# Optimization experiments

Measured on AMD Instinct MI355X. Metric: run time of the kernel, lower is better.

## Reference

```python
import jax, jax.numpy as jnp
import numpy as np

DIM, HEADS, DIM_HEAD = 512, 8, 64

def setup_inputs() -> dict:
    key = jax.random.key(0)
    ks = jax.random.split(key, 9)
    B, T = 4, 4096
    s = 1.0 / np.sqrt(DIM)
    x = jax.random.normal(ks[0], (B, T, DIM), dtype=jnp.float32)
    Wq = jax.random.uniform(ks[1], (DIM, DIM), jnp.float32, -s, s)
    Wk = jax.random.uniform(ks[2], (DIM, DIM), jnp.float32, -s, s)
    Wv = jax.random.uniform(ks[3], (DIM, DIM), jnp.float32, -s, s)
    Wp = jax.random.uniform(ks[4], (DIM, DIM), jnp.float32, -s, s)
    bq = jax.random.uniform(ks[5], (DIM,), jnp.float32, -s, s)
    bk = jax.random.uniform(ks[6], (DIM,), jnp.float32, -s, s)
    bv = jax.random.uniform(ks[7], (DIM,), jnp.float32, -s, s)
    bp = jax.random.uniform(ks[8], (DIM,), jnp.float32, -s, s)
    return {"x": x, "Wq": Wq, "bq": bq, "Wk": Wk, "bk": bk,
            "Wv": Wv, "bv": bv, "Wp": Wp, "bp": bp}

def reference(x, Wq, bq, Wk, bk, Wv, bv, Wp, bp):
    B, T, _ = x.shape
    H, D = HEADS, DIM_HEAD
    # projections -> [B, H, T, D]
    def proj(W, b):
        return (x @ W.T + b).reshape(B, T, H, D).transpose(0, 2, 1, 3)
    q = jax.nn.softmax(proj(Wq, bq), axis=-1)
    k = jax.nn.softmax(proj(Wk, bk), axis=-1)
    v = proj(Wv, bv)
    # l1 normalization: D_inv = 1 / <q, sum_t k>
    k_sum = k.sum(axis=2, keepdims=True)                 # [B,H,1,D]
    D_inv = 1.0 / (q * k_sum).sum(axis=-1, keepdims=True)  # [B,H,T,1]
    context = jnp.einsum('bhtd,bhte->bhde', k, v)        # small DxD per head
    out = jnp.einsum('bhtd,bhde->bhte', q, context) * D_inv + q
    out = out.transpose(0, 2, 1, 3).reshape(B, T, H * D)
    return out @ Wp.T + bp
```

## Files before the change

kernel.cpp:

```cpp
#include <hip/hip_runtime.h>

#define NTOK  16384
#define KDIM  512
#define NQKV  1536
#define TT    4096

using frag8   = __attribute__((ext_vector_type(8))) short;
using floatx4 = __attribute__((ext_vector_type(4))) float;

__device__ __forceinline__ unsigned short f2b(float f) {
  union { float f; unsigned u; } v; v.f = f;
  unsigned r = v.u + 0x7fffu + ((v.u >> 16) & 1u);
  return (unsigned short)(r >> 16);
}
__device__ __forceinline__ float b2f(unsigned short s) {
  union { unsigned u; float f; } v; v.u = ((unsigned)s) << 16; return v.f;
}
__device__ __forceinline__ float blo(unsigned w) {
  union { unsigned u; float f; } v; v.u = w << 16; return v.f;
}
__device__ __forceinline__ float bhi(unsigned w) {
  union { unsigned u; float f; } v; v.u = w & 0xffff0000u; return v.f;
}

__device__ __forceinline__ void gl_lds16(const void* g, void* l) {
  __builtin_amdgcn_global_load_lds((__attribute__((address_space(1))) const void*)g,
                                   (__attribute__((address_space(3))) void*)l,
                                   16, 0, 0);
}

__global__ __launch_bounds__(256) void cvt_x(const float* __restrict__ x,
                                             unsigned short* __restrict__ xb) {
  const size_t i = (size_t)blockIdx.x * 256 + threadIdx.x;
  const float4 v = ((const float4*)x)[i];
  ushort4 o;
  o.x = f2b(v.x); o.y = f2b(v.y); o.z = f2b(v.z); o.w = f2b(v.w);
  ((ushort4*)xb)[i] = o;
}

__global__ __launch_bounds__(256) void prep_weights(
    const float* __restrict__ Wq, const float* __restrict__ Wk,
    const float* __restrict__ Wv, const float* __restrict__ Wp,
    const float* __restrict__ bq, const float* __restrict__ bk,
    const float* __restrict__ bv,
    unsigned short* __restrict__ wqkv, unsigned short* __restrict__ wp,
    float* __restrict__ bias_qkv) {
  const int idx = blockIdx.x * 256 + threadIdx.x;
  if (idx < 786432) {
    const int m = idx >> 9, i = idx & 511;
    const float* W = (m < 512) ? Wq : ((m < 1024) ? Wk : Wv);
    wqkv[idx] = f2b(W[(m & 511) * 512 + i]);
    return;
  }
  const int j = idx - 786432;
  if (j < 262144) { wp[j] = f2b(Wp[j]); return; }
  const int c = j - 262144;
  if (c < 1536)
    bias_qkv[c] = (c < 512) ? bq[c] : ((c < 1024) ? bk[c - 512] : bv[c - 1024]);
}

template<int SOFT>
__global__ __launch_bounds__(256, 2) void gemm_bt(
    const unsigned short* __restrict__ A,
    const unsigned short* __restrict__ Bm,
    const float* __restrict__ bias,
    void* __restrict__ C,
    int M, int N, int K, int ldc)
{
  __shared__ unsigned short sh[2 * 128 * 32];
  unsigned short* As = sh;
  unsigned short* Bs = sh + 128 * 32;
  const int tid  = threadIdx.x;
  const int wave = tid >> 6;
  const int lane = tid & 63;
  const int quad = lane >> 4;
  const int lr   = lane & 15;
  const int bid  = ((blockIdx.x & 7) * (gridDim.x >> 3)) + (blockIdx.x >> 3);
  const int nt   = N >> 7;
  const int bn   = (bid % nt) << 7;
  const int bm   = (bid / nt) << 7;
  const int half = wave >> 1;
  const int wm   = half << 6;
  const int wn   = (wave & 1) << 6;

  floatx4 acc[4][4] = {};

  const int srow = tid >> 2;
  const int scol = (tid & 3) << 3;
  const unsigned short* Ag = A + (size_t)(bm + srow) * K + scol;
  const unsigned short* Bg = Bm + (size_t)(bn + srow) * K + scol;
  unsigned short* Al = As + (wave << 9);
  unsigned short* Bl = Bs + (wave << 9);

  for (int k0 = 0; k0 < K; k0 += 32) {
    __syncthreads();
    gl_lds16(Ag + k0, Al);
    gl_lds16(Ag + (size_t)64 * K + k0, Al + 64 * 32);
    gl_lds16(Bg + k0, Bl);
    gl_lds16(Bg + (size_t)64 * K + k0, Bl + 64 * 32);
    __syncthreads();

    frag8 af[4], bf[4];
#pragma unroll
    for (int i = 0; i < 4; i++)
      af[i] = *(const frag8*)&As[(wm + (i << 4) + lr) * 32 + (quad << 3)];
#pragma unroll
    for (int j = 0; j < 4; j++)
      bf[j] = *(const frag8*)&Bs[(wn + (j << 4) + lr) * 32 + (quad << 3)];
#pragma unroll
    for (int i = 0; i < 4; i++)
#pragma unroll
      for (int j = 0; j < 4; j++)
        acc[i][j] = __builtin_amdgcn_mfma_f32_16x16x32_bf16(af[i], bf[j], acc[i][j], 0, 0, 0);
  }

  const int ccol0 = bn + wn + lr;

#pragma unroll
  for (int j = 0; j < 4; j++) {
    const float bv = bias[ccol0 + (j << 4)];
#pragma unroll
    for (int i = 0; i < 4; i++)
#pragma unroll
      for (int r = 0; r < 4; r++)
        acc[i][j][r] += bv;
  }

  if (SOFT) {
    const int region = (bn + wn) >> 9;
    if (region < 2) {
#pragma unroll
      for (int i = 0; i < 4; i++)
#pragma unroll
        for (int r = 0; r < 4; r++) {
          float e0 = __expf(acc[i][0][r]);
          float e1 = __expf(acc[i][1][r]);
          float e2 = __expf(acc[i][2][r]);
          float e3 = __expf(acc[i][3][r]);
          float s = e0 + e1 + e2 + e3;
          s += __shfl_xor(s, 1);
          s += __shfl_xor(s, 2);
          s += __shfl_xor(s, 4);
          s += __shfl_xor(s, 8);
          const float inv = 1.f / s;
          acc[i][0][r] = e0 * inv; acc[i][1][r] = e1 * inv;
          acc[i][2][r] = e2 * inv; acc[i][3][r] = e3 * inv;
        }
    }
    unsigned short* os = sh;
#pragma unroll
    for (int p = 0; p < 2; p++) {
      __syncthreads();
      if (half == p) {
#pragma unroll
        for (int i = 0; i < 4; i++)
#pragma unroll
          for (int j = 0; j < 4; j++)
#pragma unroll
            for (int r = 0; r < 4; r++)
              os[((i << 4) + (quad << 2) + r) * 128 + wn + (j << 4) + lr] = f2b(acc[i][j][r]);
      }
      __syncthreads();
#pragma unroll
      for (int it = 0; it < 4; it++) {
        const int idx = (it << 8) + tid;
        const int row = idx >> 4;
        const int c8  = (idx & 15) << 3;
        *(uint4*)((unsigned short*)C + (size_t)(bm + (p << 6) + row) * ldc + bn + c8) =
            *(const uint4*)&os[row * 128 + c8];
      }
    }
  } else {
    const int crow0 = bm + wm + (quad << 2);
#pragma unroll
    for (int j = 0; j < 4; j++) {
      const int col = ccol0 + (j << 4);
#pragma unroll
      for (int i = 0; i < 4; i++) {
        const int row = crow0 + (i << 4);
#pragma unroll
        for (int r = 0; r < 4; r++)
          ((float*)C)[(size_t)(row + r) * ldc + col] = acc[i][j][r];
      }
    }
  }
}

__global__ __launch_bounds__(256) void kv_context(const unsigned short* __restrict__ qkv,
                                                  float* __restrict__ part,
                                                  float* __restrict__ ksp) {
  const int bid = blockIdx.x;
  const int tc  = bid & 31;
  const int bh  = bid >> 5;
  const int b   = bh >> 3, h = bh & 7;
  __shared__ float ks[16 * 64];
  __shared__ float vs[16 * 64];
  const int tid = threadIdx.x;
  const int ty = tid >> 4, tx = tid & 15;
  floatx4 acc[4] = {};
  floatx4 ksacc = {0.f, 0.f, 0.f, 0.f};

  const int si    = tid << 3;
  const int strow = si >> 7;
  const int sw    = si & 127;
  const int t0    = b * TT + tc * 128;
  const unsigned short* gcol = qkv + ((sw < 64) ? (512 + h * 64 + sw)
                                                : (1024 + h * 64 + (sw - 64)));
  float* sdst = (sw < 64) ? &ks[strow * 64 + sw] : &vs[strow * 64 + (sw - 64)];

  for (int tt = 0; tt < 128; tt += 16) {
    __syncthreads();
    const uint4 raw = *(const uint4*)(gcol + (size_t)(t0 + tt + strow) * NQKV);
    sdst[0] = blo(raw.x); sdst[1] = bhi(raw.x);
    sdst[2] = blo(raw.y); sdst[3] = bhi(raw.y);
    sdst[4] = blo(raw.z); sdst[5] = bhi(raw.z);
    sdst[6] = blo(raw.w); sdst[7] = bhi(raw.w);
    __syncthreads();
#pragma unroll
    for (int t = 0; t < 16; t++) {
      const floatx4 vb = *(const floatx4*)&vs[t * 64 + (ty << 2)];
      const floatx4 kb = *(const floatx4*)&ks[t * 64 + (tx << 2)];
      acc[0] += vb.x * kb;
      acc[1] += vb.y * kb;
      acc[2] += vb.z * kb;
      acc[3] += vb.w * kb;
    }
    ksacc += *(const floatx4*)&ks[ty * 64 + (tx << 2)];
  }
  __syncthreads();
  *(floatx4*)&vs[ty * 64 + (tx << 2)] = ksacc;
  __syncthreads();

  float* pg = part + ((size_t)(tc * 32 + bh) << 12) + (size_t)(ty << 2) * 64 + (tx << 2);
#pragma unroll
  for (int i = 0; i < 4; i++)
    *(floatx4*)(pg + i * 64) = acc[i];

  if (tid < 64) {
    float s = 0.f;
    for (int t2 = 0; t2 < 16; t2++) s += vs[t2 * 64 + tid];
    ksp[(tc * 32 + bh) * 64 + tid] = s;
  }
}

__global__ __launch_bounds__(256) void ctx_reduce(const float* __restrict__ part,
                                                  const float* __restrict__ ksp,
                                                  unsigned short* __restrict__ ctxb) {
  const int bh = blockIdx.x / 20, g = blockIdx.x % 20;
  const int row = (g << 2) + (threadIdx.x >> 6);
  const int d   = threadIdx.x & 63;
  float s = 0.f;
  if (row < 64) {
    const float* p = part + ((size_t)bh << 12) + row * 64 + d;
    for (int c = 0; c < 32; c++) s += p[(size_t)c << 17];
  } else if (row == 64) {
    const float* p = ksp + bh * 64 + d;
    for (int c = 0; c < 32; c++) s += p[c << 11];
  }
  ctxb[(size_t)bh * 5120 + (row << 6) + d] = f2b(s);
}

__global__ __launch_bounds__(256) void attn_out(const unsigned short* __restrict__ qkv,
                                                const unsigned short* __restrict__ ctxb,
                                                unsigned short* __restrict__ opre) {
  const int bid = blockIdx.x;
  const int tc = bid & 63;
  const int bh = bid >> 6;
  const int b = bh >> 3, h = bh & 7;
  const int t0 = b * TT + (tc << 6);
  __shared__ unsigned short sh[144 * 72];
  unsigned short* qs = sh;
  unsigned short* cs = sh + 64 * 72;
  unsigned short* os = cs;
  const int tid = threadIdx.x;

  for (int i = tid; i < 512; i += 256) {
    const int row = i >> 3, c8 = (i & 7) << 3;
    *(uint4*)&qs[row * 72 + c8] =
        *(const uint4*)&qkv[(size_t)(t0 + row) * NQKV + h * 64 + c8];
  }
  for (int i = tid; i < 640; i += 256) {
    const int row = i >> 3, c8 = (i & 7) << 3;
    *(uint4*)&cs[row * 72 + c8] =
        *(const uint4*)&ctxb[(size_t)bh * 5120 + (row << 6) + c8];
  }
  __syncthreads();

  const int lane = tid & 63, w = tid >> 6, quad = lane >> 4, lr = lane & 15;
  floatx4 acc[5] = {};
#pragma unroll
  for (int k2 = 0; k2 < 2; k2++) {
    const int d0 = (k2 << 5) + (quad << 3);
    const frag8 bf = *(const frag8*)&qs[((w << 4) + lr) * 72 + d0];
#pragma unroll
    for (int et = 0; et < 5; et++) {
      const frag8 af = *(const frag8*)&cs[(et * 16 + lr) * 72 + d0];
      acc[et] = __builtin_amdgcn_mfma_f32_16x16x32_bf16(af, bf, acc[et], 0, 0, 0);
    }
  }
  const float dinv = 1.f / __shfl(acc[4][0], lr);
  __syncthreads();

  const int trow = (w << 4) + lr;
#pragma unroll
  for (int et = 0; et < 4; et++)
#pragma unroll
    for (int r = 0; r < 4; r++) {
      const int e = et * 16 + (quad << 2) + r;
      const float qv = b2f(qs[trow * 72 + e]);
      os[trow * 72 + e] = f2b(acc[et][r] * dinv + qv);
    }
  __syncthreads();

  for (int i = tid; i < 512; i += 256) {
    const int row = i >> 3, c8 = (i & 7) << 3;
    *(uint4*)&opre[(size_t)(t0 + row) * KDIM + h * 64 + c8] = *(const uint4*)&os[row * 72 + c8];
  }
}

extern "C" void kernel_launch(void* const* d_in, const int* in_sizes, int n_in,
                              void* d_out, int out_size, void* d_ws, size_t ws_size,
                              hipStream_t stream) {
  (void)in_sizes; (void)n_in; (void)out_size; (void)ws_size;
  const float* x  = (const float*)d_in[0];
  const float* Wq = (const float*)d_in[1];
  const float* bq = (const float*)d_in[2];
  const float* Wk = (const float*)d_in[3];
  const float* bk = (const float*)d_in[4];
  const float* Wv = (const float*)d_in[5];
  const float* bv = (const float*)d_in[6];
  const float* Wp = (const float*)d_in[7];
  const float* bp = (const float*)d_in[8];

  char* w = (char*)d_ws;
  unsigned short* xb   = (unsigned short*)w; w += (size_t)NTOK * KDIM * 2;
  float* part          = (float*)xb;
  unsigned short* wqkv = (unsigned short*)w; w += (size_t)NQKV * KDIM * 2;
  unsigned short* wp   = (unsigned short*)w; w += (size_t)KDIM * KDIM * 2;
  float* bias_qkv      = (float*)w;          w += (size_t)NQKV * 4;
  float* ksp           = (float*)w;          w += (size_t)1024 * 64 * 4;
  unsigned short* ctxb = (unsigned short*)w; w += (size_t)32 * 80 * 64 * 2;
  unsigned short* qkv  = (unsigned short*)w; w += (size_t)NTOK * NQKV * 2;
  unsigned short* opre = (unsigned short*)w; w += (size_t)NTOK * KDIM * 2;

  cvt_x<<<8192, 256, 0, stream>>>(x, xb);
  prep_weights<<<4102, 256, 0, stream>>>(Wq, Wk, Wv, Wp, bq, bk, bv, wqkv, wp, bias_qkv);
  gemm_bt<1><<<(NTOK / 128) * (NQKV / 128), 256, 0, stream>>>(
      xb, wqkv, bias_qkv, qkv, NTOK, NQKV, KDIM, NQKV);
  kv_context<<<1024, 256, 0, stream>>>(qkv, part, ksp);
  ctx_reduce<<<640, 256, 0, stream>>>(part, ksp, ctxb);
  attn_out<<<2048, 256, 0, stream>>>(qkv, ctxb, opre);
  gemm_bt<0><<<(NTOK / 128) * (KDIM / 128), 256, 0, stream>>>(
      opre, wp, bp, d_out, NTOK, KDIM, KDIM, KDIM);
}
```

Before: 192.7 us.

## Enlarge QKV GEMM tile, async-load K/V in bf16, vectorize reduce, drop LDS staging in attn_out

The QKV GEMM moves to a 256x128 block tile in which each wave computes 64x128, so the softmax covers two heads per wave and each LDS-staged tile is reused more. kv_context now fetches K/V straight into LDS as bf16 with global_load_lds and converts at use time, instead of converting to fp32 in registers first. ctx_reduce uses float4 loads with a quarter of the blocks. attn_out reads Q and the context directly from global memory without staging them in LDS, and reorders blocks so that heads are interleaved. gemm_out hardcodes its dimensions. The larger accumulator raises register pressure, and the bf16 rounding of the output before the q add changes precision slightly.

```diff
diff --git a/kernel.cpp b/kernel.cpp
--- a/kernel.cpp
+++ b/kernel.cpp
@@ -15,12 +15,6 @@
 }
 __device__ __forceinline__ float b2f(unsigned short s) {
   union { unsigned u; float f; } v; v.u = ((unsigned)s) << 16; return v.f;
-}
-__device__ __forceinline__ float blo(unsigned w) {
-  union { unsigned u; float f; } v; v.u = w << 16; return v.f;
-}
-__device__ __forceinline__ float bhi(unsigned w) {
-  union { unsigned u; float f; } v; v.u = w & 0xffff0000u; return v.f;
 }
 
 __device__ __forceinline__ void gl_lds16(const void* g, void* l) {
@@ -59,13 +53,254 @@
     bias_qkv[c] = (c < 512) ? bq[c] : ((c < 1024) ? bk[c - 512] : bv[c - 1024]);
 }
 
-template<int SOFT>
-__global__ __launch_bounds__(256, 2) void gemm_bt(
+__global__ __launch_bounds__(256, 2) void gemm_qkv(
     const unsigned short* __restrict__ A,
     const unsigned short* __restrict__ Bm,
     const float* __restrict__ bias,
-    void* __restrict__ C,
-    int M, int N, int K, int ldc)
+    unsigned short* __restrict__ C)
+{
+  __shared__ unsigned short sh[128 * 128];
+  unsigned short* As = sh;
+  unsigned short* Bs = sh + 256 * 32;
+  const int tid  = threadIdx.x;
+  const int wave = tid >> 6;
+  const int lane = tid & 63;
+  const int quad = lane >> 4;
+  const int lr   = lane & 15;
+  const int bid  = ((blockIdx.x & 7) * 96) + (blockIdx.x >> 3);
+  const int bn   = (bid % 12) << 7;
+  const int bm   = (bid / 12) << 8;
+  const int wm   = wave << 6;
+
+  floatx4 acc[4][8] = {};
+
+  const int srow = tid >> 2;
+  const int scol = (tid & 3) << 3;
+  const unsigned short* Ag = A + (size_t)(bm + srow) * 512 + scol;
+  const unsigned short* Bg = Bm + (size_t)(bn + srow) * 512 + scol;
+  unsigned short* Al = As + (wave << 9);
+  unsigned short* Bl = Bs + (wave << 9);
+
+  for (int k0 = 0; k0 < 512; k0 += 32) {
+    __syncthreads();
+    gl_lds16(Ag + k0, Al);
+    gl_lds16(Ag + 64 * 512 + k0, Al + 64 * 32);
+    gl_lds16(Ag + 128 * 512 + k0, Al + 128 * 32);
+    gl_lds16(Ag + 192 * 512 + k0, Al + 192 * 32);
+    gl_lds16(Bg + k0, Bl);
+    gl_lds16(Bg + 64 * 512 + k0, Bl + 64 * 32);
+    __syncthreads();
+
+    frag8 af[4], bf[8];
+#pragma unroll
+    for (int i = 0; i < 4; i++)
+      af[i] = *(const frag8*)&As[(wm + (i << 4) + lr) * 32 + (quad << 3)];
+#pragma unroll
+    for (int j = 0; j < 8; j++)
+      bf[j] = *(const frag8*)&Bs[((j << 4) + lr) * 32 + (quad << 3)];
+#pragma unroll
+    for (int i = 0; i < 4; i++)
+#pragma unroll
+      for (int j = 0; j < 8; j++)
+        acc[i][j] = __builtin_amdgcn_mfma_f32_16x16x32_bf16(af[i], bf[j], acc[i][j], 0, 0, 0);
+  }
+
+  const int ccol0 = bn + lr;
+#pragma unroll
+  for (int j = 0; j < 8; j++) {
+    const float bv = bias[ccol0 + (j << 4)];
+#pragma unroll
+    for (int i = 0; i < 4; i++)
+#pragma unroll
+      for (int r = 0; r < 4; r++)
+        acc[i][j][r] += bv;
+  }
+
+  const int region = bn >> 9;
+  if (region < 2) {
+#pragma unroll
+    for (int i = 0; i < 4; i++)
+#pragma unroll
+      for (int r = 0; r < 4; r++) {
+        float e0 = __expf(acc[i][0][r]);
+        float e1 = __expf(acc[i][1][r]);
+        float e2 = __expf(acc[i][2][r]);
+        float e3 = __expf(acc[i][3][r]);
+        float e4 = __expf(acc[i][4][r]);
+        float e5 = __expf(acc[i][5][r]);
+        float e6 = __expf(acc[i][6][r]);
+        float e7 = __expf(acc[i][7][r]);
+        float sl = e0 + e1 + e2 + e3;
+        float sg = e4 + e5 + e6 + e7;
+        sl += __shfl_xor(sl, 1); sl += __shfl_xor(sl, 2);
+        sl += __shfl_xor(sl, 4); sl += __shfl_xor(sl, 8);
+        sg += __shfl_xor(sg, 1); sg += __shfl_xor(sg, 2);
+        sg += __shfl_xor(sg, 4); sg += __shfl_xor(sg, 8);
+        const float il = 1.f / sl, ig = 1.f / sg;
+        acc[i][0][r] = e0 * il; acc[i][1][r] = e1 * il;
+        acc[i][2][r] = e2 * il; acc[i][3][r] = e3 * il;
+        acc[i][4][r] = e4 * ig; acc[i][5][r] = e5 * ig;
+        acc[i][6][r] = e6 * ig; acc[i][7][r] = e7 * ig;
+      }
+  }
+
+  unsigned short* os = sh;
+#pragma unroll
+  for (int p = 0; p < 2; p++) {
+    __syncthreads();
+    if ((wave >> 1) == p) {
+      const int rb = (wave & 1) << 6;
+#pragma unroll
+      for (int i = 0; i < 4; i++)
+#pragma unroll
+        for (int j = 0; j < 8; j++)
+#pragma unroll
+          for (int r = 0; r < 4; r++)
+            os[(rb + (i << 4) + (quad << 2) + r) * 128 + (j << 4) + lr] = f2b(acc[i][j][r]);
+    }
+    __syncthreads();
+#pragma unroll
+    for (int it = 0; it < 8; it++) {
+      const int idx = (it << 8) + tid;
+      const int row = idx >> 4;
+      const int c8  = (idx & 15) << 3;
+      *(uint4*)(C + (size_t)(bm + (p << 7) + row) * NQKV + bn + c8) =
+          *(const uint4*)&os[row * 128 + c8];
+    }
+  }
+}
+
+__global__ __launch_bounds__(256) void kv_context(const unsigned short* __restrict__ qkv,
+                                                  float* __restrict__ part,
+                                                  float* __restrict__ ksp) {
+  const int bid = blockIdx.x;
+  const int tc  = bid & 31;
+  const int bh  = bid >> 5;
+  const int b   = bh >> 3, h = bh & 7;
+  __shared__ unsigned short kb16[16 * 64];
+  __shared__ unsigned short vb16[16 * 64];
+  __shared__ float ksred[16 * 64];
+  const int tid = threadIdx.x;
+  const int wave = tid >> 6;
+  const int lane = tid & 63;
+  const int ty = tid >> 4, tx = tid & 15;
+  floatx4 acc[4] = {};
+  floatx4 ksacc = {0.f, 0.f, 0.f, 0.f};
+
+  const int t0 = b * TT + tc * 128;
+  const int kvsel = wave >> 1;
+  const int rowb  = (wave & 1) << 3;
+  const unsigned short* gsrc = qkv + (size_t)(t0 + rowb + (lane >> 3)) * NQKV
+                               + 512 + (kvsel << 9) + h * 64 + ((lane & 7) << 3);
+  unsigned short* ldst = (kvsel ? vb16 : kb16) + (rowb << 6);
+
+  for (int tt = 0; tt < 128; tt += 16) {
+    __syncthreads();
+    gl_lds16(gsrc + (size_t)tt * NQKV, ldst);
+    __syncthreads();
+#pragma unroll
+    for (int t = 0; t < 16; t++) {
+      const ushort4 kr = *(const ushort4*)&kb16[t * 64 + (tx << 2)];
+      const ushort4 vr = *(const ushort4*)&vb16[t * 64 + (ty << 2)];
+      floatx4 kf;
+      kf.x = b2f(kr.x); kf.y = b2f(kr.y); kf.z = b2f(kr.z); kf.w = b2f(kr.w);
+      acc[0] += b2f(vr.x) * kf;
+      acc[1] += b2f(vr.y) * kf;
+      acc[2] += b2f(vr.z) * kf;
+      acc[3] += b2f(vr.w) * kf;
+    }
+    const ushort4 kk = *(const ushort4*)&kb16[ty * 64 + (tx << 2)];
+    ksacc.x += b2f(kk.x); ksacc.y += b2f(kk.y);
+    ksacc.z += b2f(kk.z); ksacc.w += b2f(kk.w);
+  }
+  __syncthreads();
+  *(floatx4*)&ksred[ty * 64 + (tx << 2)] = ksacc;
+  __syncthreads();
+
+  float* pg = part + ((size_t)(tc * 32 + bh) << 12) + (size_t)(ty << 2) * 64 + (tx << 2);
+#pragma unroll
+  for (int i = 0; i < 4; i++)
+    *(floatx4*)(pg + i * 64) = acc[i];
+
+  if (tid < 64) {
+    float s = 0.f;
+    for (int t2 = 0; t2 < 16; t2++) s += ksred[t2 * 64 + tid];
+    ksp[(tc * 32 + bh) * 64 + tid] = s;
+  }
+}
+
+__global__ __launch_bounds__(256) void ctx_reduce(const float* __restrict__ part,
+                                                  const float* __restrict__ ksp,
+                                                  unsigned short* __restrict__ ctxb) {
+  const int bh = blockIdx.x / 5, g = blockIdx.x % 5;
+  const int row = (g << 4) + (threadIdx.x >> 4);
+  const int d0  = (threadIdx.x & 15) << 2;
+  floatx4 s = {0.f, 0.f, 0.f, 0.f};
+  if (row < 64) {
+    const float* p = part + ((size_t)bh << 12) + row * 64 + d0;
+    for (int c = 0; c < 32; c++)
+      s += *(const floatx4*)(p + ((size_t)c << 17));
+  } else if (row == 64) {
+    const float* p = ksp + bh * 64 + d0;
+    for (int c = 0; c < 32; c++)
+      s += *(const floatx4*)(p + (c << 11));
+  }
+  ushort4 o;
+  o.x = f2b(s.x); o.y = f2b(s.y); o.z = f2b(s.z); o.w = f2b(s.w);
+  *(ushort4*)&ctxb[(size_t)bh * 5120 + (row << 6) + d0] = o;
+}
+
+__global__ __launch_bounds__(256) void attn_out(const unsigned short* __restrict__ qkv,
+                                                const unsigned short* __restrict__ ctxb,
+                                                unsigned short* __restrict__ opre) {
+  const int tc = blockIdx.x >> 5;
+  const int bh = blockIdx.x & 31;
+  const int b = bh >> 3, h = bh & 7;
+  const int t0 = b * TT + (tc << 6);
+  __shared__ unsigned short os[64 * 72];
+  const int tid = threadIdx.x;
+  const int lane = tid & 63, w = tid >> 6, quad = lane >> 4, lr = lane & 15;
+
+  floatx4 acc[5] = {};
+  const unsigned short* qbase = qkv + (size_t)(t0 + (w << 4) + lr) * NQKV + h * 64 + (quad << 3);
+  const unsigned short* cbase = ctxb + (size_t)bh * 5120 + (quad << 3);
+#pragma unroll
+  for (int k2 = 0; k2 < 2; k2++) {
+    const frag8 bfr = *(const frag8*)(qbase + (k2 << 5));
+#pragma unroll
+    for (int et = 0; et < 5; et++) {
+      const frag8 afr = *(const frag8*)(cbase + (((et << 4) + lr) << 6) + (k2 << 5));
+      acc[et] = __builtin_amdgcn_mfma_f32_16x16x32_bf16(afr, bfr, acc[et], 0, 0, 0);
+    }
+  }
+  const float dinv = 1.f / __shfl(acc[4][0], lr);
+
+  const int trow = (w << 4) + lr;
+#pragma unroll
+  for (int et = 0; et < 4; et++)
+#pragma unroll
+    for (int r = 0; r < 4; r++)
+      os[trow * 72 + (et << 4) + (quad << 2) + r] = f2b(acc[et][r] * dinv);
+  __syncthreads();
+
+  for (int i = tid; i < 512; i += 256) {
+    const int row = i >> 3, c8 = (i & 7) << 3;
+    const uint4 qraw = *(const uint4*)&qkv[(size_t)(t0 + row) * NQKV + h * 64 + c8];
+    const uint4 ov   = *(const uint4*)&os[row * 72 + c8];
+    const unsigned short* qp = (const unsigned short*)&qraw;
+    const unsigned short* op = (const unsigned short*)&ov;
+    unsigned short o8[8];
+#pragma unroll
+    for (int jj = 0; jj < 8; jj++) o8[jj] = f2b(b2f(op[jj]) + b2f(qp[jj]));
+    *(uint4*)&opre[(size_t)(t0 + row) * KDIM + h * 64 + c8] = *(const uint4*)o8;
+  }
+}
+
+__global__ __launch_bounds__(256, 2) void gemm_out(
+    const unsigned short* __restrict__ A,
+    const unsigned short* __restrict__ Bm,
+    const float* __restrict__ bias,
+    float* __restrict__ C)
 {
   __shared__ unsigned short sh[2 * 128 * 32];
   unsigned short* As = sh;
@@ -75,29 +310,27 @@
   const int lane = tid & 63;
   const int quad = lane >> 4;
   const int lr   = lane & 15;
-  const int bid  = ((blockIdx.x & 7) * (gridDim.x >> 3)) + (blockIdx.x >> 3);
-  const int nt   = N >> 7;
-  const int bn   = (bid % nt) << 7;
-  const int bm   = (bid / nt) << 7;
-  const int half = wave >> 1;
-  const int wm   = half << 6;
+  const int bid  = ((blockIdx.x & 7) * 64) + (blockIdx.x >> 3);
+  const int bn   = (bid & 3) << 7;
+  const int bm   = (bid >> 2) << 7;
+  const int wm   = (wave >> 1) << 6;
   const int wn   = (wave & 1) << 6;
 
   floatx4 acc[4][4] = {};
 
   const int srow = tid >> 2;
   const int scol = (tid & 3) << 3;
-  const unsigned short* Ag = A + (size_t)(bm + srow) * K + scol;
-  const unsigned short* Bg = Bm + (size_t)(bn + srow) * K + scol;
+  const unsigned short* Ag = A + (size_t)(bm + srow) * 512 + scol;
+  const unsigned short* Bg = Bm + (size_t)(bn + srow) * 512 + scol;
   unsigned short* Al = As + (wave << 9);
   unsigned short* Bl = Bs + (wave << 9);
 
-  for (int k0 = 0; k0 < K; k0 += 32) {
+  for (int k0 = 0; k0 < 512; k0 += 32) {
     __syncthreads();
     gl_lds16(Ag + k0, Al);
-    gl_lds16(Ag + (size_t)64 * K + k0, Al + 64 * 32);
+    gl_lds16(Ag + 64 * 512 + k0, Al + 64 * 32);
     gl_lds16(Bg + k0, Bl);
-    gl_lds16(Bg + (size_t)64 * K + k0, Bl + 64 * 32);
+    gl_lds16(Bg + 64 * 512 + k0, Bl + 64 * 32);
     __syncthreads();
 
     frag8 af[4], bf[4];
@@ -114,207 +347,19 @@
         acc[i][j] = __builtin_amdgcn_mfma_f32_16x16x32_bf16(af[i], bf[j], acc[i][j], 0, 0, 0);
   }
 
+  const int crow0 = bm + wm + (quad << 2);
   const int ccol0 = bn + wn + lr;
-
 #pragma unroll
   for (int j = 0; j < 4; j++) {
-    const float bv = bias[ccol0 + (j << 4)];
-#pragma unroll
-    for (int i = 0; i < 4; i++)
+    const int col = ccol0 + (j << 4);
+    const float bv = bias[col];
+#pragma unroll
+    for (int i = 0; i < 4; i++) {
+      const int row = crow0 + (i << 4);
 #pragma unroll
       for (int r = 0; r < 4; r++)
-        acc[i][j][r] += bv;
-  }
-
-  if (SOFT) {
-    const int region = (bn + wn) >> 9;
-    if (region < 2) {
-#pragma unroll
-      for (int i = 0; i < 4; i++)
-#pragma unroll
-        for (int r = 0; r < 4; r++) {
-          float e0 = __expf(acc[i][0][r]);
-          float e1 = __expf(acc[i][1][r]);
-          float e2 = __expf(acc[i][2][r]);
-          float e3 = __expf(acc[i][3][r]);
-          float s = e0 + e1 + e2 + e3;
-          s += __shfl_xor(s, 1);
-          s += __shfl_xor(s, 2);
-          s += __shfl_xor(s, 4);
-          s += __shfl_xor(s, 8);
-          const float inv = 1.f / s;
-          acc[i][0][r] = e0 * inv; acc[i][1][r] = e1 * inv;
-          acc[i][2][r] = e2 * inv; acc[i][3][r] = e3 * inv;
-        }
-    }
-    unsigned short* os = sh;
-#pragma unroll
-    for (int p = 0; p < 2; p++) {
-      __syncthreads();
-      if (half == p) {
-#pragma unroll
-        for (int i = 0; i < 4; i++)
-#pragma unroll
-          for (int j = 0; j < 4; j++)
-#pragma unroll
-            for (int r = 0; r < 4; r++)
-              os[((i << 4) + (quad << 2) + r) * 128 + wn + (j << 4) + lr] = f2b(acc[i][j][r]);
-      }
-      __syncthreads();
-#pragma unroll
-      for (int it = 0; it < 4; it++) {
-        const int idx = (it << 8) + tid;
-        const int row = idx >> 4;
-        const int c8  = (idx & 15) << 3;
-        *(uint4*)((unsigned short*)C + (size_t)(bm + (p << 6) + row) * ldc + bn + c8) =
-            *(const uint4*)&os[row * 128 + c8];
-      }
-    }
-  } else {
-    const int crow0 = bm + wm + (quad << 2);
-#pragma unroll
-    for (int j = 0; j < 4; j++) {
-      const int col = ccol0 + (j << 4);
-#pragma unroll
-      for (int i = 0; i < 4; i++) {
-        const int row = crow0 + (i << 4);
-#pragma unroll
-        for (int r = 0; r < 4; r++)
-          ((float*)C)[(size_t)(row + r) * ldc + col] = acc[i][j][r];
-      }
-    }
-  }
-}
-
-__global__ __launch_bounds__(256) void kv_context(const unsigned short* __restrict__ qkv,
-                                                  float* __restrict__ part,
-                                                  float* __restrict__ ksp) {
-  const int bid = blockIdx.x;
-  const int tc  = bid & 31;
-  const int bh  = bid >> 5;
-  const int b   = bh >> 3, h = bh & 7;
-  __shared__ float ks[16 * 64];
-  __shared__ float vs[16 * 64];
-  const int tid = threadIdx.x;
-  const int ty = tid >> 4, tx = tid & 15;
-  floatx4 acc[4] = {};
-  floatx4 ksacc = {0.f, 0.f, 0.f, 0.f};
-
-  const int si    = tid << 3;
-  const int strow = si >> 7;
-  const int sw    = si & 127;
-  const int t0    = b * TT + tc * 128;
-  const unsigned short* gcol = qkv + ((sw < 64) ? (512 + h * 64 + sw)
-                                                : (1024 + h * 64 + (sw - 64)));
-  float* sdst = (sw < 64) ? &ks[strow * 64 + sw] : &vs[strow * 64 + (sw - 64)];
-
-  for (int tt = 0; tt < 128; tt += 16) {
-    __syncthreads();
-    const uint4 raw = *(const uint4*)(gcol + (size_t)(t0 + tt + strow) * NQKV);
-    sdst[0] = blo(raw.x); sdst[1] = bhi(raw.x);
-    sdst[2] = blo(raw.y); sdst[3] = bhi(raw.y);
-    sdst[4] = blo(raw.z); sdst[5] = bhi(raw.z);
-    sdst[6] = blo(raw.w); sdst[7] = bhi(raw.w);
-    __syncthreads();
-#pragma unroll
-    for (int t = 0; t < 16; t++) {
-      const floatx4 vb = *(const floatx4*)&vs[t * 64 + (ty << 2)];
-      const floatx4 kb = *(const floatx4*)&ks[t * 64 + (tx << 2)];
-      acc[0] += vb.x * kb;
-      acc[1] += vb.y * kb;
-      acc[2] += vb.z * kb;
-      acc[3] += vb.w * kb;
-    }
-    ksacc += *(const floatx4*)&ks[ty * 64 + (tx << 2)];
-  }
-  __syncthreads();
-  *(floatx4*)&vs[ty * 64 + (tx << 2)] = ksacc;
-  __syncthreads();
-
-  float* pg = part + ((size_t)(tc * 32 + bh) << 12) + (size_t)(ty << 2) * 64 + (tx << 2);
-#pragma unroll
-  for (int i = 0; i < 4; i++)
-    *(floatx4*)(pg + i * 64) = acc[i];
-
-  if (tid < 64) {
-    float s = 0.f;
-    for (int t2 = 0; t2 < 16; t2++) s += vs[t2 * 64 + tid];
-    ksp[(tc * 32 + bh) * 64 + tid] = s;
-  }
-}
-
-__global__ __launch_bounds__(256) void ctx_reduce(const float* __restrict__ part,
-                                                  const float* __restrict__ ksp,
-                                                  unsigned short* __restrict__ ctxb) {
-  const int bh = blockIdx.x / 20, g = blockIdx.x % 20;
-  const int row = (g << 2) + (threadIdx.x >> 6);
-  const int d   = threadIdx.x & 63;
-  float s = 0.f;
-  if (row < 64) {
-    const float* p = part + ((size_t)bh << 12) + row * 64 + d;
-    for (int c = 0; c < 32; c++) s += p[(size_t)c << 17];
-  } else if (row == 64) {
-    const float* p = ksp + bh * 64 + d;
-    for (int c = 0; c < 32; c++) s += p[c << 11];
-  }
-  ctxb[(size_t)bh * 5120 + (row << 6) + d] = f2b(s);
-}
-
-__global__ __launch_bounds__(256) void attn_out(const unsigned short* __restrict__ qkv,
-                                                const unsigned short* __restrict__ ctxb,
-                                                unsigned short* __restrict__ opre) {
-  const int bid = blockIdx.x;
-  const int tc = bid & 63;
-  const int bh = bid >> 6;
-  const int b = bh >> 3, h = bh & 7;
-  const int t0 = b * TT + (tc << 6);
-  __shared__ unsigned short sh[144 * 72];
-  unsigned short* qs = sh;
-  unsigned short* cs = sh + 64 * 72;
-  unsigned short* os = cs;
-  const int tid = threadIdx.x;
-
-  for (int i = tid; i < 512; i += 256) {
-    const int row = i >> 3, c8 = (i & 7) << 3;
-    *(uint4*)&qs[row * 72 + c8] =
-        *(const uint4*)&qkv[(size_t)(t0 + row) * NQKV + h * 64 + c8];
-  }
-  for (int i = tid; i < 640; i += 256) {
-    const int row = i >> 3, c8 = (i & 7) << 3;
-    *(uint4*)&cs[row * 72 + c8] =
-        *(const uint4*)&ctxb[(size_t)bh * 5120 + (row << 6) + c8];
-  }
-  __syncthreads();
-
-  const int lane = tid & 63, w = tid >> 6, quad = lane >> 4, lr = lane & 15;
-  floatx4 acc[5] = {};
-#pragma unroll
-  for (int k2 = 0; k2 < 2; k2++) {
-    const int d0 = (k2 << 5) + (quad << 3);
-    const frag8 bf = *(const frag8*)&qs[((w << 4) + lr) * 72 + d0];
-#pragma unroll
-    for (int et = 0; et < 5; et++) {
-      const frag8 af = *(const frag8*)&cs[(et * 16 + lr) * 72 + d0];
-      acc[et] = __builtin_amdgcn_mfma_f32_16x16x32_bf16(af, bf, acc[et], 0, 0, 0);
-    }
-  }
-  const float dinv = 1.f / __shfl(acc[4][0], lr);
-  __syncthreads();
-
-  const int trow = (w << 4) + lr;
-#pragma unroll
-  for (int et = 0; et < 4; et++)
-#pragma unroll
-    for (int r = 0; r < 4; r++) {
-      const int e = et * 16 + (quad << 2) + r;
-      const float qv = b2f(qs[trow * 72 + e]);
-      os[trow * 72 + e] = f2b(acc[et][r] * dinv + qv);
-    }
-  __syncthreads();
-
-  for (int i = tid; i < 512; i += 256) {
-    const int row = i >> 3, c8 = (i & 7) << 3;
-    *(uint4*)&opre[(size_t)(t0 + row) * KDIM + h * 64 + c8] = *(const uint4*)&os[row * 72 + c8];
+        C[(size_t)(row + r) * 512 + col] = acc[i][j][r] + bv;
+    }
   }
 }
 
@@ -345,11 +390,9 @@
 
   cvt_x<<<8192, 256, 0, stream>>>(x, xb);
   prep_weights<<<4102, 256, 0, stream>>>(Wq, Wk, Wv, Wp, bq, bk, bv, wqkv, wp, bias_qkv);
-  gemm_bt<1><<<(NTOK / 128) * (NQKV / 128), 256, 0, stream>>>(
-      xb, wqkv, bias_qkv, qkv, NTOK, NQKV, KDIM, NQKV);
+  gemm_qkv<<<768, 256, 0, stream>>>(xb, wqkv, bias_qkv, qkv);
   kv_context<<<1024, 256, 0, stream>>>(qkv, part, ksp);
-  ctx_reduce<<<640, 256, 0, stream>>>(part, ksp, ctxb);
+  ctx_reduce<<<160, 256, 0, stream>>>(part, ksp, ctxb);
   attn_out<<<2048, 256, 0, stream>>>(qkv, ctxb, opre);
-  gemm_bt<0><<<(NTOK / 128) * (KDIM / 128), 256, 0, stream>>>(
-      opre, wp, bp, d_out, NTOK, KDIM, KDIM, KDIM);
-}
+  gemm_out<<<512, 256, 0, stream>>>(opre, wp, bp, (float*)d_out);
+}
```

After: 205.5 us. +6.6%, slower.

## Stream K/V directly from global in kv_context, vectorize ctx_reduce, raise gemm occupancy

Applied to the files above, without the earlier changes.

kv_context drops its LDS staging and syncthreads. Each thread now loads its own 4-wide K and V bf16 slices straight from global memory and accumulates the outer product and the k-sum in registers. ctx_reduce becomes float4-vectorized with a quarter of the blocks, attn_out's block index mapping is changed to interleave heads, and the gemm launch bounds ask for 4 blocks per SM. These aim to cut sync overhead, raise memory throughput and improve occupancy. The costs are redundant global loads across threads in kv_context and register pressure in the gemm.

```diff
diff --git a/kernel.cpp b/kernel.cpp
--- a/kernel.cpp
+++ b/kernel.cpp
@@ -15,12 +15,6 @@
 }
 __device__ __forceinline__ float b2f(unsigned short s) {
   union { unsigned u; float f; } v; v.u = ((unsigned)s) << 16; return v.f;
-}
-__device__ __forceinline__ float blo(unsigned w) {
-  union { unsigned u; float f; } v; v.u = w << 16; return v.f;
-}
-__device__ __forceinline__ float bhi(unsigned w) {
-  union { unsigned u; float f; } v; v.u = w & 0xffff0000u; return v.f;
 }
 
 __device__ __forceinline__ void gl_lds16(const void* g, void* l) {
@@ -60,7 +54,7 @@
 }
 
 template<int SOFT>
-__global__ __launch_bounds__(256, 2) void gemm_bt(
+__global__ __launch_bounds__(256, 4) void gemm_bt(
     const unsigned short* __restrict__ A,
     const unsigned short* __restrict__ Bm,
     const float* __restrict__ bias,
@@ -189,83 +183,66 @@
 __global__ __launch_bounds__(256) void kv_context(const unsigned short* __restrict__ qkv,
                                                   float* __restrict__ part,
                                                   float* __restrict__ ksp) {
-  const int bid = blockIdx.x;
-  const int tc  = bid & 31;
-  const int bh  = bid >> 5;
+  const int tc  = blockIdx.x & 31;
+  const int bh  = blockIdx.x >> 5;
   const int b   = bh >> 3, h = bh & 7;
-  __shared__ float ks[16 * 64];
-  __shared__ float vs[16 * 64];
   const int tid = threadIdx.x;
   const int ty = tid >> 4, tx = tid & 15;
   floatx4 acc[4] = {};
   floatx4 ksacc = {0.f, 0.f, 0.f, 0.f};
 
-  const int si    = tid << 3;
-  const int strow = si >> 7;
-  const int sw    = si & 127;
-  const int t0    = b * TT + tc * 128;
-  const unsigned short* gcol = qkv + ((sw < 64) ? (512 + h * 64 + sw)
-                                                : (1024 + h * 64 + (sw - 64)));
-  float* sdst = (sw < 64) ? &ks[strow * 64 + sw] : &vs[strow * 64 + (sw - 64)];
-
-  for (int tt = 0; tt < 128; tt += 16) {
-    __syncthreads();
-    const uint4 raw = *(const uint4*)(gcol + (size_t)(t0 + tt + strow) * NQKV);
-    sdst[0] = blo(raw.x); sdst[1] = bhi(raw.x);
-    sdst[2] = blo(raw.y); sdst[3] = bhi(raw.y);
-    sdst[4] = blo(raw.z); sdst[5] = bhi(raw.z);
-    sdst[6] = blo(raw.w); sdst[7] = bhi(raw.w);
-    __syncthreads();
-#pragma unroll
-    for (int t = 0; t < 16; t++) {
-      const floatx4 vb = *(const floatx4*)&vs[t * 64 + (ty << 2)];
-      const floatx4 kb = *(const floatx4*)&ks[t * 64 + (tx << 2)];
-      acc[0] += vb.x * kb;
-      acc[1] += vb.y * kb;
-      acc[2] += vb.z * kb;
-      acc[3] += vb.w * kb;
-    }
-    ksacc += *(const floatx4*)&ks[ty * 64 + (tx << 2)];
-  }
-  __syncthreads();
-  *(floatx4*)&vs[ty * 64 + (tx << 2)] = ksacc;
-  __syncthreads();
+  const int t0 = b * TT + tc * 128;
+  const unsigned short* kp = qkv + (size_t)t0 * NQKV + 512 + h * 64 + (tx << 2);
+  const unsigned short* vp = qkv + (size_t)t0 * NQKV + 1024 + h * 64 + (ty << 2);
+
+#pragma unroll 8
+  for (int t = 0; t < 128; t++) {
+    const ushort4 kr = *(const ushort4*)(kp + (size_t)t * NQKV);
+    const ushort4 vr = *(const ushort4*)(vp + (size_t)t * NQKV);
+    floatx4 kf;
+    kf.x = b2f(kr.x); kf.y = b2f(kr.y); kf.z = b2f(kr.z); kf.w = b2f(kr.w);
+    acc[0] += b2f(vr.x) * kf;
+    acc[1] += b2f(vr.y) * kf;
+    acc[2] += b2f(vr.z) * kf;
+    acc[3] += b2f(vr.w) * kf;
+    ksacc += kf;
+  }
 
   float* pg = part + ((size_t)(tc * 32 + bh) << 12) + (size_t)(ty << 2) * 64 + (tx << 2);
 #pragma unroll
   for (int i = 0; i < 4; i++)
     *(floatx4*)(pg + i * 64) = acc[i];
 
-  if (tid < 64) {
-    float s = 0.f;
-    for (int t2 = 0; t2 < 16; t2++) s += vs[t2 * 64 + tid];
-    ksp[(tc * 32 + bh) * 64 + tid] = s;
-  }
+  if (ty == 0)
+    *(floatx4*)&ksp[(tc * 32 + bh) * 64 + (tx << 2)] = ksacc;
 }
 
 __global__ __launch_bounds__(256) void ctx_reduce(const float* __restrict__ part,
                                                   const float* __restrict__ ksp,
                                                   unsigned short* __restrict__ ctxb) {
-  const int bh = blockIdx.x / 20, g = blockIdx.x % 20;
-  const int row = (g << 2) + (threadIdx.x >> 6);
-  const int d   = threadIdx.x & 63;
-  float s = 0.f;
+  const int bh = blockIdx.x / 5, g = blockIdx.x % 5;
+  const int row = (g << 4) + (threadIdx.x >> 4);
+  const int d0  = (threadIdx.x & 15) << 2;
+  floatx4 s = {0.f, 0.f, 0.f, 0.f};
   if (row < 64) {
-    const float* p = part + ((size_t)bh << 12) + row * 64 + d;
-    for (int c = 0; c < 32; c++) s += p[(size_t)c << 17];
+    const float* p = part + ((size_t)bh << 12) + row * 64 + d0;
+    for (int c = 0; c < 32; c++)
+      s += *(const floatx4*)(p + ((size_t)c << 17));
   } else if (row == 64) {
-    const float* p = ksp + bh * 64 + d;
-    for (int c = 0; c < 32; c++) s += p[c << 11];
-  }
-  ctxb[(size_t)bh * 5120 + (row << 6) + d] = f2b(s);
+    const float* p = ksp + bh * 64 + d0;
+    for (int c = 0; c < 32; c++)
+      s += *(const floatx4*)(p + (c << 11));
+  }
+  ushort4 o;
+  o.x = f2b(s.x); o.y = f2b(s.y); o.z = f2b(s.z); o.w = f2b(s.w);
+  *(ushort4*)&ctxb[(size_t)bh * 5120 + (row << 6) + d0] = o;
 }
 
 __global__ __launch_bounds__(256) void attn_out(const unsigned short* __restrict__ qkv,
                                                 const unsigned short* __restrict__ ctxb,
                                                 unsigned short* __restrict__ opre) {
-  const int bid = blockIdx.x;
-  const int tc = bid & 63;
-  const int bh = bid >> 6;
+  const int tc = blockIdx.x >> 5;
+  const int bh = blockIdx.x & 31;
   const int b = bh >> 3, h = bh & 7;
   const int t0 = b * TT + (tc << 6);
   __shared__ unsigned short sh[144 * 72];
@@ -348,7 +325,7 @@
   gemm_bt<1><<<(NTOK / 128) * (NQKV / 128), 256, 0, stream>>>(
       xb, wqkv, bias_qkv, qkv, NTOK, NQKV, KDIM, NQKV);
   kv_context<<<1024, 256, 0, stream>>>(qkv, part, ksp);
-  ctx_reduce<<<640, 256, 0, stream>>>(part, ksp, ctxb);
+  ctx_reduce<<<160, 256, 0, stream>>>(part, ksp, ctxb);
   attn_out<<<2048, 256, 0, stream>>>(qkv, ctxb, opre);
   gemm_bt<0><<<(NTOK / 128) * (KDIM / 128), 256, 0, stream>>>(
       opre, wp, bp, d_out, NTOK, KDIM, KDIM, KDIM);
```

Measured after the change: 205.1 us. +6.4%, slower.

## Merge conversion kernels, deepen GEMM K-tile with XOR swizzle, vectorize reductions

Applied to the files above, without the earlier changes.

Fuses the x and weight conversion kernels into a single launch. Doubles the GEMM K-step to 64 with an XOR-swizzled LDS layout, which halves the barrier count per tile and is meant to avoid LDS bank conflicts on fragment reads. Vectorizes the LDS stores in kv_context and the loads and stores in ctx_reduce, which now runs with fewer blocks. Reorders the attn_out block mapping so the heads of one token chunk run next to each other. The larger LDS tile raises shared memory per block, which may limit occupancy.

```diff
diff --git a/kernel.cpp b/kernel.cpp
--- a/kernel.cpp
+++ b/kernel.cpp
@@ -29,23 +29,25 @@
                                    16, 0, 0);
 }
 
-__global__ __launch_bounds__(256) void cvt_x(const float* __restrict__ x,
-                                             unsigned short* __restrict__ xb) {
-  const size_t i = (size_t)blockIdx.x * 256 + threadIdx.x;
-  const float4 v = ((const float4*)x)[i];
-  ushort4 o;
-  o.x = f2b(v.x); o.y = f2b(v.y); o.z = f2b(v.z); o.w = f2b(v.w);
-  ((ushort4*)xb)[i] = o;
-}
-
-__global__ __launch_bounds__(256) void prep_weights(
+__global__ __launch_bounds__(256) void cvt_all(
+    const float* __restrict__ x,
     const float* __restrict__ Wq, const float* __restrict__ Wk,
     const float* __restrict__ Wv, const float* __restrict__ Wp,
     const float* __restrict__ bq, const float* __restrict__ bk,
     const float* __restrict__ bv,
+    unsigned short* __restrict__ xb,
     unsigned short* __restrict__ wqkv, unsigned short* __restrict__ wp,
     float* __restrict__ bias_qkv) {
-  const int idx = blockIdx.x * 256 + threadIdx.x;
+  const int blk = blockIdx.x;
+  if (blk < 8192) {
+    const size_t i = (size_t)blk * 256 + threadIdx.x;
+    const float4 v = ((const float4*)x)[i];
+    ushort4 o;
+    o.x = f2b(v.x); o.y = f2b(v.y); o.z = f2b(v.z); o.w = f2b(v.w);
+    ((ushort4*)xb)[i] = o;
+    return;
+  }
+  const int idx = (blk - 8192) * 256 + threadIdx.x;
   if (idx < 786432) {
     const int m = idx >> 9, i = idx & 511;
     const float* W = (m < 512) ? Wq : ((m < 1024) ? Wk : Wv);
@@ -67,14 +69,15 @@
     void* __restrict__ C,
     int M, int N, int K, int ldc)
 {
-  __shared__ unsigned short sh[2 * 128 * 32];
+  __shared__ unsigned short sh[2 * 128 * 64];
   unsigned short* As = sh;
-  unsigned short* Bs = sh + 128 * 32;
+  unsigned short* Bs = sh + 128 * 64;
   const int tid  = threadIdx.x;
   const int wave = tid >> 6;
   const int lane = tid & 63;
   const int quad = lane >> 4;
   const int lr   = lane & 15;
+  const int sw7  = lr & 7;
   const int bid  = ((blockIdx.x & 7) * (gridDim.x >> 3)) + (blockIdx.x >> 3);
   const int nt   = N >> 7;
   const int bn   = (bid % nt) << 7;
@@ -85,33 +88,41 @@
 
   floatx4 acc[4][4] = {};
 
-  const int srow = tid >> 2;
-  const int scol = (tid & 3) << 3;
+  const int srow = tid >> 3;
+  const int scol = ((tid & 7) ^ ((tid >> 3) & 7)) << 3;
   const unsigned short* Ag = A + (size_t)(bm + srow) * K + scol;
   const unsigned short* Bg = Bm + (size_t)(bn + srow) * K + scol;
   unsigned short* Al = As + (wave << 9);
   unsigned short* Bl = Bs + (wave << 9);
 
-  for (int k0 = 0; k0 < K; k0 += 32) {
+  for (int k0 = 0; k0 < K; k0 += 64) {
     __syncthreads();
-    gl_lds16(Ag + k0, Al);
-    gl_lds16(Ag + (size_t)64 * K + k0, Al + 64 * 32);
-    gl_lds16(Bg + k0, Bl);
-    gl_lds16(Bg + (size_t)64 * K + k0, Bl + 64 * 32);
+    gl_lds16(Ag + k0,                    Al);
+    gl_lds16(Ag + (size_t)32 * K + k0,   Al + 2048);
+    gl_lds16(Ag + (size_t)64 * K + k0,   Al + 4096);
+    gl_lds16(Ag + (size_t)96 * K + k0,   Al + 6144);
+    gl_lds16(Bg + k0,                    Bl);
+    gl_lds16(Bg + (size_t)32 * K + k0,   Bl + 2048);
+    gl_lds16(Bg + (size_t)64 * K + k0,   Bl + 4096);
+    gl_lds16(Bg + (size_t)96 * K + k0,   Bl + 6144);
     __syncthreads();
 
-    frag8 af[4], bf[4];
-#pragma unroll
-    for (int i = 0; i < 4; i++)
-      af[i] = *(const frag8*)&As[(wm + (i << 4) + lr) * 32 + (quad << 3)];
-#pragma unroll
-    for (int j = 0; j < 4; j++)
-      bf[j] = *(const frag8*)&Bs[(wn + (j << 4) + lr) * 32 + (quad << 3)];
-#pragma unroll
-    for (int i = 0; i < 4; i++)
+#pragma unroll
+    for (int kk = 0; kk < 2; kk++) {
+      const int coff = ((((kk << 2) + quad) ^ sw7) << 3);
+      frag8 af[4], bf[4];
+#pragma unroll
+      for (int i = 0; i < 4; i++)
+        af[i] = *(const frag8*)&As[(wm + (i << 4) + lr) * 64 + coff];
 #pragma unroll
       for (int j = 0; j < 4; j++)
-        acc[i][j] = __builtin_amdgcn_mfma_f32_16x16x32_bf16(af[i], bf[j], acc[i][j], 0, 0, 0);
+        bf[j] = *(const frag8*)&Bs[(wn + (j << 4) + lr) * 64 + coff];
+#pragma unroll
+      for (int i = 0; i < 4; i++)
+#pragma unroll
+        for (int j = 0; j < 4; j++)
+          acc[i][j] = __builtin_amdgcn_mfma_f32_16x16x32_bf16(af[i], bf[j], acc[i][j], 0, 0, 0);
+    }
   }
 
   const int ccol0 = bn + wn + lr;
@@ -211,10 +222,10 @@
   for (int tt = 0; tt < 128; tt += 16) {
     __syncthreads();
     const uint4 raw = *(const uint4*)(gcol + (size_t)(t0 + tt + strow) * NQKV);
-    sdst[0] = blo(raw.x); sdst[1] = bhi(raw.x);
-    sdst[2] = blo(raw.y); sdst[3] = bhi(raw.y);
-    sdst[4] = blo(raw.z); sdst[5] = bhi(raw.z);
-    sdst[6] = blo(raw.w); sdst[7] = bhi(raw.w);
+    const floatx4 f0 = {blo(raw.x), bhi(raw.x), blo(raw.y), bhi(raw.y)};
+    const floatx4 f1 = {blo(raw.z), bhi(raw.z), blo(raw.w), bhi(raw.w)};
+    *(floatx4*)sdst = f0;
+    *(floatx4*)(sdst + 4) = f1;
     __syncthreads();
 #pragma unroll
     for (int t = 0; t < 16; t++) {
@@ -246,26 +257,29 @@
 __global__ __launch_bounds__(256) void ctx_reduce(const float* __restrict__ part,
                                                   const float* __restrict__ ksp,
                                                   unsigned short* __restrict__ ctxb) {
-  const int bh = blockIdx.x / 20, g = blockIdx.x % 20;
-  const int row = (g << 2) + (threadIdx.x >> 6);
-  const int d   = threadIdx.x & 63;
-  float s = 0.f;
+  const int bh = blockIdx.x / 5, g = blockIdx.x % 5;
+  const int row = (g << 4) + (threadIdx.x >> 4);
+  const int d0  = (threadIdx.x & 15) << 2;
+  floatx4 s = {0.f, 0.f, 0.f, 0.f};
   if (row < 64) {
-    const float* p = part + ((size_t)bh << 12) + row * 64 + d;
-    for (int c = 0; c < 32; c++) s += p[(size_t)c << 17];
+    const float* p = part + ((size_t)bh << 12) + row * 64 + d0;
+    for (int c = 0; c < 32; c++)
+      s += *(const floatx4*)(p + ((size_t)c << 17));
   } else if (row == 64) {
-    const float* p = ksp + bh * 64 + d;
-    for (int c = 0; c < 32; c++) s += p[c << 11];
-  }
-  ctxb[(size_t)bh * 5120 + (row << 6) + d] = f2b(s);
+    const float* p = ksp + bh * 64 + d0;
+    for (int c = 0; c < 32; c++)
+      s += *(const floatx4*)(p + (c << 11));
+  }
+  ushort4 o;
+  o.x = f2b(s.x); o.y = f2b(s.y); o.z = f2b(s.z); o.w = f2b(s.w);
+  *(ushort4*)&ctxb[(size_t)bh * 5120 + (row << 6) + d0] = o;
 }
 
 __global__ __launch_bounds__(256) void attn_out(const unsigned short* __restrict__ qkv,
                                                 const unsigned short* __restrict__ ctxb,
                                                 unsigned short* __restrict__ opre) {
-  const int bid = blockIdx.x;
-  const int tc = bid & 63;
-  const int bh = bid >> 6;
+  const int tc = blockIdx.x >> 5;
+  const int bh = blockIdx.x & 31;
   const int b = bh >> 3, h = bh & 7;
   const int t0 = b * TT + (tc << 6);
   __shared__ unsigned short sh[144 * 72];
@@ -343,12 +357,12 @@
   unsigned short* qkv  = (unsigned short*)w; w += (size_t)NTOK * NQKV * 2;
   unsigned short* opre = (unsigned short*)w; w += (size_t)NTOK * KDIM * 2;
 
-  cvt_x<<<8192, 256, 0, stream>>>(x, xb);
-  prep_weights<<<4102, 256, 0, stream>>>(Wq, Wk, Wv, Wp, bq, bk, bv, wqkv, wp, bias_qkv);
+  cvt_all<<<12294, 256, 0, stream>>>(x, Wq, Wk, Wv, Wp, bq, bk, bv,
+                                     xb, wqkv, wp, bias_qkv);
   gemm_bt<1><<<(NTOK / 128) * (NQKV / 128), 256, 0, stream>>>(
       xb, wqkv, bias_qkv, qkv, NTOK, NQKV, KDIM, NQKV);
   kv_context<<<1024, 256, 0, stream>>>(qkv, part, ksp);
-  ctx_reduce<<<640, 256, 0, stream>>>(part, ksp, ctxb);
+  ctx_reduce<<<160, 256, 0, stream>>>(part, ksp, ctxb);
   attn_out<<<2048, 256, 0, stream>>>(qkv, ctxb, opre);
   gemm_bt<0><<<(NTOK / 128) * (KDIM / 128), 256, 0, stream>>>(
       opre, wp, bp, d_out, NTOK, KDIM, KDIM, KDIM);
```

After: 177.8 us. -7.7%, faster.
